# Kernel optimization log

Hardware: AMD Instinct MI355X
Metric: run time of the kernel (lower is better)

## Reference

```python
import jax, jax.numpy as jnp
import numpy as np

NUM_ENT = 7
DIM_ENT = 4
NEMBED_HALF = 128  # nembed_ctx / 2
BATCH = 16384


def setup_inputs() -> dict:
    key = jax.random.key(0)
    k1, k2, k3, k4, k5 = jax.random.split(key, 5)
    ctx = jax.random.normal(k1, (NUM_ENT * DIM_ENT, BATCH), dtype=jnp.float32)
    init = 0.01
    w_prop = jax.random.uniform(k2, (DIM_ENT, NEMBED_HALF), jnp.float32, -init, init)
    b_prop = jax.random.uniform(k3, (NEMBED_HALF,), jnp.float32, -init, init)
    w_rel = jax.random.uniform(k4, (DIM_ENT + 1, NEMBED_HALF), jnp.float32, -init, init)
    b_rel = jax.random.uniform(k5, (NEMBED_HALF,), jnp.float32, -init, init)
    return {"ctx": ctx, "w_prop": w_prop, "b_prop": b_prop, "w_rel": w_rel, "b_rel": b_rel}


def reference(ctx, w_prop, b_prop, w_rel, b_rel):
    # ctx: [num_ent*dim_ent, B] -> ents: [B, num_ent, dim_ent]
    ents = ctx.T.reshape(-1, NUM_ENT, DIM_ENT)
    # property embedding: Linear + ReLU (dropout = identity at inference)
    prop_emb = jax.nn.relu(jnp.einsum('bnd,dh->bnh', ents, w_prop) + b_prop)
    # pairwise diffs [B, i, j, d] and euclidean distance over first two coords
    diffs = ents[:, :, None, :] - ents[:, None, :, :]
    dist = jnp.sqrt(diffs[..., 0] ** 2 + diffs[..., 1] ** 2)  # [B, i, j]
    feats = jnp.concatenate([diffs, dist[..., None]], axis=-1)  # [B, i, j, dim_ent+1]
    rel = jax.nn.relu(jnp.einsum('bijd,dh->bijh', feats, w_rel) + b_rel)
    # original loops skip i == j: zero the diagonal before summing over j
    off_diag = (1.0 - jnp.eye(NUM_ENT, dtype=rel.dtype))[None, :, :, None]
    rel_emb = jnp.sum(rel * off_diag, axis=2)  # [B, num_ent, H]
    return jnp.concatenate([prop_emb, rel_emb], axis=2)  # [B, num_ent, 2H]
```

## Files before the change

### kernel.cpp

```cpp
#include <hip/hip_runtime.h>

#define NUM_ENT 7
#define DIM_ENT 4
#define H 128
#define OUTC (2 * H)
#define BPB 8

typedef float f32x4 __attribute__((ext_vector_type(4)));

__global__ __launch_bounds__(256) void ace_kernel(
    const float* __restrict__ ctx,
    const float* __restrict__ w_prop,
    const float* __restrict__ b_prop,
    const float* __restrict__ w_rel,
    const float* __restrict__ b_rel,
    float* __restrict__ out,
    int B)
{
    __shared__ float s_ents[BPB][NUM_ENT * DIM_ENT];

    const int tid = threadIdx.x;
    const int b0 = blockIdx.x * BPB;

    if (tid < BPB * NUM_ENT * DIM_ENT) {
        const int k  = tid >> 3;
        const int bb = tid & 7;
        s_ents[bb][k] = ctx[(size_t)k * B + (b0 + bb)];
    }
    __syncthreads();

    const int w    = tid >> 6;
    const int lane = tid & 63;
    const int bb   = w * 2 + (lane >> 5);
    const int c4   = (lane & 31) << 2;
    float* outb = out + (size_t)(b0 + bb) * (NUM_ENT * OUTC);

    f32x4 e[NUM_ENT];
#pragma unroll
    for (int n = 0; n < NUM_ENT; ++n)
        e[n] = *(const f32x4*)(&s_ents[bb][n * DIM_ENT]);

    {
        const f32x4 w0 = *(const f32x4*)(w_prop + 0 * H + c4);
        const f32x4 w1 = *(const f32x4*)(w_prop + 1 * H + c4);
        const f32x4 w2 = *(const f32x4*)(w_prop + 2 * H + c4);
        const f32x4 w3 = *(const f32x4*)(w_prop + 3 * H + c4);
        const f32x4 bp = *(const f32x4*)(b_prop + c4);
#pragma unroll
        for (int n = 0; n < NUM_ENT; ++n) {
            const float e0 = e[n].x, e1 = e[n].y, e2 = e[n].z, e3 = e[n].w;
            f32x4 a;
            a.x = fmaxf(bp.x + e0 * w0.x + e1 * w1.x + e2 * w2.x + e3 * w3.x, 0.f);
            a.y = fmaxf(bp.y + e0 * w0.y + e1 * w1.y + e2 * w2.y + e3 * w3.y, 0.f);
            a.z = fmaxf(bp.z + e0 * w0.z + e1 * w1.z + e2 * w2.z + e3 * w3.z, 0.f);
            a.w = fmaxf(bp.w + e0 * w0.w + e1 * w1.w + e2 * w2.w + e3 * w3.w, 0.f);
            __builtin_nontemporal_store(a, (f32x4*)(outb + n * OUTC + c4));
        }
    }

    {
        const f32x4 w0 = *(const f32x4*)(w_rel + 0 * H + c4);
        const f32x4 w1 = *(const f32x4*)(w_rel + 1 * H + c4);
        const f32x4 w2 = *(const f32x4*)(w_rel + 2 * H + c4);
        const f32x4 w3 = *(const f32x4*)(w_rel + 3 * H + c4);
        const f32x4 w4 = *(const f32x4*)(w_rel + 4 * H + c4);
        const f32x4 br = *(const f32x4*)(b_rel + c4);
#pragma unroll
        for (int i = 0; i < NUM_ENT; ++i) {
            f32x4 acc = {0.f, 0.f, 0.f, 0.f};
#pragma unroll
            for (int j = 0; j < NUM_ENT; ++j) {
                if (j == i) continue;
                const float dx = e[i].x - e[j].x;
                const float dy = e[i].y - e[j].y;
                const float dz = e[i].z - e[j].z;
                const float dv = e[i].w - e[j].w;
                const float d  = __builtin_amdgcn_sqrtf(dx * dx + dy * dy);
                acc.x += fmaxf(br.x + dx * w0.x + dy * w1.x + dz * w2.x + dv * w3.x + d * w4.x, 0.f);
                acc.y += fmaxf(br.y + dx * w0.y + dy * w1.y + dz * w2.y + dv * w3.y + d * w4.y, 0.f);
                acc.z += fmaxf(br.z + dx * w0.z + dy * w1.z + dz * w2.z + dv * w3.z + d * w4.z, 0.f);
                acc.w += fmaxf(br.w + dx * w0.w + dy * w1.w + dz * w2.w + dv * w3.w + d * w4.w, 0.f);
            }
            __builtin_nontemporal_store(acc, (f32x4*)(outb + i * OUTC + H + c4));
        }
    }
}

extern "C" void kernel_launch(void* const* d_in, const int* in_sizes, int n_in,
                              void* d_out, int out_size, void* d_ws, size_t ws_size,
                              hipStream_t stream) {
    const float* ctx    = (const float*)d_in[0];
    const float* w_prop = (const float*)d_in[1];
    const float* b_prop = (const float*)d_in[2];
    const float* w_rel  = (const float*)d_in[3];
    const float* b_rel  = (const float*)d_in[4];
    float* out = (float*)d_out;

    const int B = in_sizes[0] / (NUM_ENT * DIM_ENT);
    const int nb = (B + BPB - 1) / BPB;
    ace_kernel<<<nb, 256, 0, stream>>>(ctx, w_prop, b_prop, w_rel, b_rel, out, B);
}
```

Measured before the change: 140.9 us.

## Process 16 batch rows per block with 8 channels per thread

Doubles the batch rows per block to 16 and gives each thread 8 output channels in two strided groups of 4, so 16 threads cover one row instead of 32. Each block launches half as many times, and the entity differences and sqrt computed per pair are shared across twice as many channels, cutting redundant work. Nontemporal stores become ordinary stores, and register use per thread goes up.

```diff
diff --git a/kernel.cpp b/kernel.cpp
--- a/kernel.cpp
+++ b/kernel.cpp
@@ -4,7 +4,7 @@
 #define DIM_ENT 4
 #define H 128
 #define OUTC (2 * H)
-#define BPB 8
+#define BPB 16
 
 typedef float f32x4 __attribute__((ext_vector_type(4)));
 
@@ -22,17 +22,17 @@
     const int tid = threadIdx.x;
     const int b0 = blockIdx.x * BPB;
 
-    if (tid < BPB * NUM_ENT * DIM_ENT) {
-        const int k  = tid >> 3;
-        const int bb = tid & 7;
+#pragma unroll
+    for (int t = tid; t < BPB * NUM_ENT * DIM_ENT; t += 256) {
+        const int k  = t >> 4;
+        const int bb = t & 15;
         s_ents[bb][k] = ctx[(size_t)k * B + (b0 + bb)];
     }
     __syncthreads();
 
-    const int w    = tid >> 6;
-    const int lane = tid & 63;
-    const int bb   = w * 2 + (lane >> 5);
-    const int c4   = (lane & 31) << 2;
+    const int sub = tid & 15;
+    const int bb  = tid >> 4;
+    const int c0  = sub << 2;
     float* outb = out + (size_t)(b0 + bb) * (NUM_ENT * OUTC);
 
     f32x4 e[NUM_ENT];
@@ -41,33 +41,44 @@
         e[n] = *(const f32x4*)(&s_ents[bb][n * DIM_ENT]);
 
     {
-        const f32x4 w0 = *(const f32x4*)(w_prop + 0 * H + c4);
-        const f32x4 w1 = *(const f32x4*)(w_prop + 1 * H + c4);
-        const f32x4 w2 = *(const f32x4*)(w_prop + 2 * H + c4);
-        const f32x4 w3 = *(const f32x4*)(w_prop + 3 * H + c4);
-        const f32x4 bp = *(const f32x4*)(b_prop + c4);
+        f32x4 wp[DIM_ENT][2], bp[2];
+#pragma unroll
+        for (int f = 0; f < DIM_ENT; ++f) {
+            wp[f][0] = *(const f32x4*)(w_prop + f * H + c0);
+            wp[f][1] = *(const f32x4*)(w_prop + f * H + c0 + 64);
+        }
+        bp[0] = *(const f32x4*)(b_prop + c0);
+        bp[1] = *(const f32x4*)(b_prop + c0 + 64);
 #pragma unroll
         for (int n = 0; n < NUM_ENT; ++n) {
             const float e0 = e[n].x, e1 = e[n].y, e2 = e[n].z, e3 = e[n].w;
-            f32x4 a;
-            a.x = fmaxf(bp.x + e0 * w0.x + e1 * w1.x + e2 * w2.x + e3 * w3.x, 0.f);
-            a.y = fmaxf(bp.y + e0 * w0.y + e1 * w1.y + e2 * w2.y + e3 * w3.y, 0.f);
-            a.z = fmaxf(bp.z + e0 * w0.z + e1 * w1.z + e2 * w2.z + e3 * w3.z, 0.f);
-            a.w = fmaxf(bp.w + e0 * w0.w + e1 * w1.w + e2 * w2.w + e3 * w3.w, 0.f);
-            __builtin_nontemporal_store(a, (f32x4*)(outb + n * OUTC + c4));
+#pragma unroll
+            for (int q = 0; q < 2; ++q) {
+                f32x4 a = bp[q];
+                a += e0 * wp[0][q];
+                a += e1 * wp[1][q];
+                a += e2 * wp[2][q];
+                a += e3 * wp[3][q];
+                a.x = fmaxf(a.x, 0.f); a.y = fmaxf(a.y, 0.f);
+                a.z = fmaxf(a.z, 0.f); a.w = fmaxf(a.w, 0.f);
+                *(f32x4*)(outb + n * OUTC + c0 + q * 64) = a;
+            }
         }
     }
 
     {
-        const f32x4 w0 = *(const f32x4*)(w_rel + 0 * H + c4);
-        const f32x4 w1 = *(const f32x4*)(w_rel + 1 * H + c4);
-        const f32x4 w2 = *(const f32x4*)(w_rel + 2 * H + c4);
-        const f32x4 w3 = *(const f32x4*)(w_rel + 3 * H + c4);
-        const f32x4 w4 = *(const f32x4*)(w_rel + 4 * H + c4);
-        const f32x4 br = *(const f32x4*)(b_rel + c4);
+        f32x4 wr[DIM_ENT + 1][2], br[2];
+#pragma unroll
+        for (int f = 0; f < DIM_ENT + 1; ++f) {
+            wr[f][0] = *(const f32x4*)(w_rel + f * H + c0);
+            wr[f][1] = *(const f32x4*)(w_rel + f * H + c0 + 64);
+        }
+        br[0] = *(const f32x4*)(b_rel + c0);
+        br[1] = *(const f32x4*)(b_rel + c0 + 64);
 #pragma unroll
         for (int i = 0; i < NUM_ENT; ++i) {
-            f32x4 acc = {0.f, 0.f, 0.f, 0.f};
+            f32x4 acc0 = {0.f, 0.f, 0.f, 0.f};
+            f32x4 acc1 = {0.f, 0.f, 0.f, 0.f};
 #pragma unroll
             for (int j = 0; j < NUM_ENT; ++j) {
                 if (j == i) continue;
@@ -76,12 +87,23 @@
                 const float dz = e[i].z - e[j].z;
                 const float dv = e[i].w - e[j].w;
                 const float d  = __builtin_amdgcn_sqrtf(dx * dx + dy * dy);
-                acc.x += fmaxf(br.x + dx * w0.x + dy * w1.x + dz * w2.x + dv * w3.x + d * w4.x, 0.f);
-                acc.y += fmaxf(br.y + dx * w0.y + dy * w1.y + dz * w2.y + dv * w3.y + d * w4.y, 0.f);
-                acc.z += fmaxf(br.z + dx * w0.z + dy * w1.z + dz * w2.z + dv * w3.z + d * w4.z, 0.f);
-                acc.w += fmaxf(br.w + dx * w0.w + dy * w1.w + dz * w2.w + dv * w3.w + d * w4.w, 0.f);
+                {
+                    f32x4 t = br[0];
+                    t += dx * wr[0][0]; t += dy * wr[1][0]; t += dz * wr[2][0];
+                    t += dv * wr[3][0]; t += d  * wr[4][0];
+                    acc0.x += fmaxf(t.x, 0.f); acc0.y += fmaxf(t.y, 0.f);
+                    acc0.z += fmaxf(t.z, 0.f); acc0.w += fmaxf(t.w, 0.f);
+                }
+                {
+                    f32x4 t = br[1];
+                    t += dx * wr[0][1]; t += dy * wr[1][1]; t += dz * wr[2][1];
+                    t += dv * wr[3][1]; t += d  * wr[4][1];
+                    acc1.x += fmaxf(t.x, 0.f); acc1.y += fmaxf(t.y, 0.f);
+                    acc1.z += fmaxf(t.z, 0.f); acc1.w += fmaxf(t.w, 0.f);
+                }
             }
-            __builtin_nontemporal_store(acc, (f32x4*)(outb + i * OUTC + H + c4));
+            *(f32x4*)(outb + i * OUTC + H + c0)      = acc0;
+            *(f32x4*)(outb + i * OUTC + H + c0 + 64) = acc1;
         }
     }
 }
```

New measurement: 129.7 us. 7.9% less time.

## Cut register pressure with rolled loops, LDS reloads and occupancy launch bound

Applied to the files above, without the earlier changes.

Adds a min-blocks-per-CU hint to launch bounds and stops keeping all seven entity vectors in registers, reloading them from shared memory inside rolled loops. The arithmetic is rewritten in vector form, and the nontemporal output stores become plain stores. The aim is more resident waves per CU to hide the latency of a store-heavy kernel. The cost is extra LDS reads and loop overhead, and the output writes lose their nontemporal cache hint.

```diff
diff --git a/kernel.cpp b/kernel.cpp
--- a/kernel.cpp
+++ b/kernel.cpp
@@ -8,7 +8,7 @@
 
 typedef float f32x4 __attribute__((ext_vector_type(4)));
 
-__global__ __launch_bounds__(256) void ace_kernel(
+__global__ __launch_bounds__(256, 8) void ace_kernel(
     const float* __restrict__ ctx,
     const float* __restrict__ w_prop,
     const float* __restrict__ b_prop,
@@ -34,27 +34,26 @@
     const int bb   = w * 2 + (lane >> 5);
     const int c4   = (lane & 31) << 2;
     float* outb = out + (size_t)(b0 + bb) * (NUM_ENT * OUTC);
+    const float* se = &s_ents[bb][0];
 
-    f32x4 e[NUM_ENT];
-#pragma unroll
-    for (int n = 0; n < NUM_ENT; ++n)
-        e[n] = *(const f32x4*)(&s_ents[bb][n * DIM_ENT]);
+    const f32x4 vzero = {0.f, 0.f, 0.f, 0.f};
 
     {
-        const f32x4 w0 = *(const f32x4*)(w_prop + 0 * H + c4);
-        const f32x4 w1 = *(const f32x4*)(w_prop + 1 * H + c4);
-        const f32x4 w2 = *(const f32x4*)(w_prop + 2 * H + c4);
-        const f32x4 w3 = *(const f32x4*)(w_prop + 3 * H + c4);
-        const f32x4 bp = *(const f32x4*)(b_prop + c4);
-#pragma unroll
+        const f32x4 wp0 = *(const f32x4*)(w_prop + 0 * H + c4);
+        const f32x4 wp1 = *(const f32x4*)(w_prop + 1 * H + c4);
+        const f32x4 wp2 = *(const f32x4*)(w_prop + 2 * H + c4);
+        const f32x4 wp3 = *(const f32x4*)(w_prop + 3 * H + c4);
+        const f32x4 bp  = *(const f32x4*)(b_prop + c4);
+#pragma unroll 1
         for (int n = 0; n < NUM_ENT; ++n) {
-            const float e0 = e[n].x, e1 = e[n].y, e2 = e[n].z, e3 = e[n].w;
-            f32x4 a;
-            a.x = fmaxf(bp.x + e0 * w0.x + e1 * w1.x + e2 * w2.x + e3 * w3.x, 0.f);
-            a.y = fmaxf(bp.y + e0 * w0.y + e1 * w1.y + e2 * w2.y + e3 * w3.y, 0.f);
-            a.z = fmaxf(bp.z + e0 * w0.z + e1 * w1.z + e2 * w2.z + e3 * w3.z, 0.f);
-            a.w = fmaxf(bp.w + e0 * w0.w + e1 * w1.w + e2 * w2.w + e3 * w3.w, 0.f);
-            __builtin_nontemporal_store(a, (f32x4*)(outb + n * OUTC + c4));
+            const f32x4 en = *(const f32x4*)(se + n * DIM_ENT);
+            f32x4 a = bp;
+            a += en.x * wp0;
+            a += en.y * wp1;
+            a += en.z * wp2;
+            a += en.w * wp3;
+            a = __builtin_elementwise_max(a, vzero);
+            *(f32x4*)(outb + n * OUTC + c4) = a;
         }
     }
 
@@ -65,23 +64,28 @@
         const f32x4 w3 = *(const f32x4*)(w_rel + 3 * H + c4);
         const f32x4 w4 = *(const f32x4*)(w_rel + 4 * H + c4);
         const f32x4 br = *(const f32x4*)(b_rel + c4);
-#pragma unroll
+#pragma unroll 1
         for (int i = 0; i < NUM_ENT; ++i) {
-            f32x4 acc = {0.f, 0.f, 0.f, 0.f};
-#pragma unroll
+            const f32x4 ei = *(const f32x4*)(se + i * DIM_ENT);
+            f32x4 acc = vzero;
+#pragma unroll 1
             for (int j = 0; j < NUM_ENT; ++j) {
                 if (j == i) continue;
-                const float dx = e[i].x - e[j].x;
-                const float dy = e[i].y - e[j].y;
-                const float dz = e[i].z - e[j].z;
-                const float dv = e[i].w - e[j].w;
+                const f32x4 ej = *(const f32x4*)(se + j * DIM_ENT);
+                const float dx = ei.x - ej.x;
+                const float dy = ei.y - ej.y;
+                const float dz = ei.z - ej.z;
+                const float dv = ei.w - ej.w;
                 const float d  = __builtin_amdgcn_sqrtf(dx * dx + dy * dy);
-                acc.x += fmaxf(br.x + dx * w0.x + dy * w1.x + dz * w2.x + dv * w3.x + d * w4.x, 0.f);
-                acc.y += fmaxf(br.y + dx * w0.y + dy * w1.y + dz * w2.y + dv * w3.y + d * w4.y, 0.f);
-                acc.z += fmaxf(br.z + dx * w0.z + dy * w1.z + dz * w2.z + dv * w3.z + d * w4.z, 0.f);
-                acc.w += fmaxf(br.w + dx * w0.w + dy * w1.w + dz * w2.w + dv * w3.w + d * w4.w, 0.f);
+                f32x4 t = br;
+                t += dx * w0;
+                t += dy * w1;
+                t += dz * w2;
+                t += dv * w3;
+                t += d  * w4;
+                acc += __builtin_elementwise_max(t, vzero);
             }
-            __builtin_nontemporal_store(acc, (f32x4*)(outb + i * OUTC + H + c4));
+            *(f32x4*)(outb + i * OUTC + H + c4) = acc;
         }
     }
 }
```

Result: faster. 135.4 us (-3.9%).
